# Performance work log

Measured on AMD Instinct MI355X. Metric: run time of the kernel, lower is better.

The kernel has to match this reference:

```python
import jax, jax.numpy as jnp
import numpy as np


def _round_ste(v):
    # straight-through rounding (typical LinearQuantize autograd STE)
    return v + jax.lax.stop_gradient(jnp.round(v) - v)


def setup_inputs() -> dict:
    key = jax.random.key(0)
    k1, k2, k3 = jax.random.split(key, 3)
    tokens, d_in, d_out = 8192, 2048, 2048
    x = jax.random.uniform(k1, (tokens, d_in), dtype=jnp.float32)  # non-negative acts
    weight = jax.random.normal(k2, (d_out, d_in), dtype=jnp.float32) * 0.02
    bias = jax.random.normal(k3, (d_out,), dtype=jnp.float32) * 0.02
    return {"x": x, "weight": weight, "bias": bias, "weight_bit": 8}


def reference(x, weight, bias, weight_bit):
    n = 2 ** weight_bit
    # stats computed on detached data (x.data/w.data in torch)
    wd = jax.lax.stop_gradient(weight)
    w_min = wd.min(axis=1)                      # [out]
    w_max = wd.max(axis=1)                      # [out]
    x_max = jax.lax.stop_gradient(x).max()
    scale_x = (n - 1) / jnp.clip(x_max, 1e-8)
    # activation quantization: round(scale_x * x - 0)
    q_x = _round_ste(scale_x * x)               # [T, in]
    # per-channel asymmetric weight quant (quantize_int)
    scale_w = (n - 1) / jnp.clip(w_max - w_min, 1e-8)   # [out]
    zp_w = scale_w * w_min                      # [out]
    q_w = _round_ste(scale_w[:, None] * weight - zp_w[:, None])  # [out, in]
    # bias quantized with combined scale, then clamped
    q_b = jnp.clip(_round_ste(bias * scale_w * scale_x), -n - 1, n)  # [out]
    # fake-int GEMM + zero-point correction + rescale
    mult = jnp.einsum('ti,oi->to', q_x, q_w) + q_b      # [T, out]
    res = mult + zp_w * q_x.sum(-1, keepdims=True)
    return res / scale_x / scale_w
```

## Files before the change

### kernel.cpp

```cpp
#include <hip/hip_runtime.h>
#include <stdint.h>

typedef __attribute__((ext_vector_type(4))) int i32x4;

__device__ inline float wave_max(float v){ for(int o=32;o;o>>=1) v=fmaxf(v,__shfl_xor(v,o)); return v; }
__device__ inline float wave_min(float v){ for(int o=32;o;o>>=1) v=fminf(v,__shfl_xor(v,o)); return v; }
__device__ inline int   wave_sum(int v){ for(int o=32;o;o>>=1) v+=__shfl_xor(v,o); return v; }

__device__ inline void gload16(const void* g, void* l){
  __builtin_amdgcn_global_load_lds((const __attribute__((address_space(1))) char*)g,
                                   (__attribute__((address_space(3))) char*)l, 16, 0, 0);
}

__global__ void k_xmax_partial(const float* __restrict__ x, long long n4,
                               float* __restrict__ partials){
  long long i = (long long)blockIdx.x*blockDim.x + threadIdx.x;
  long long stride = (long long)gridDim.x*blockDim.x;
  const float4* x4 = (const float4*)x;
  float m = 0.f;
  for(; i < n4; i += stride){
    float4 v = x4[i];
    m = fmaxf(m, fmaxf(fmaxf(v.x,v.y),fmaxf(v.z,v.w)));
  }
  m = wave_max(m);
  __shared__ float sm[4];
  int lane = threadIdx.x & 63, wid = threadIdx.x >> 6;
  if(lane==0) sm[wid] = m;
  __syncthreads();
  if(threadIdx.x==0)
    partials[blockIdx.x] = fmaxf(fmaxf(sm[0],sm[1]),fmaxf(sm[2],sm[3]));
}

__global__ void k_xmax_final(const float* __restrict__ partials, int nPart,
                             uint32_t* __restrict__ xmax_bits){
  float m = 0.f;
  for(int i = threadIdx.x; i < nPart; i += 256) m = fmaxf(m, partials[i]);
  m = wave_max(m);
  __shared__ float sm[4];
  int lane = threadIdx.x & 63, wid = threadIdx.x >> 6;
  if(lane==0) sm[wid] = m;
  __syncthreads();
  if(threadIdx.x==0)
    *xmax_bits = __float_as_uint(fmaxf(fmaxf(sm[0],sm[1]),fmaxf(sm[2],sm[3])));
}

__global__ void k_wstat(const float* __restrict__ w, const float* __restrict__ bias,
                        const int* __restrict__ wbit, const uint32_t* __restrict__ xmax_bits,
                        float* __restrict__ scale_w, float* __restrict__ zp_w,
                        float* __restrict__ winv,
                        int* __restrict__ cint, char* __restrict__ qw, int din){
  int row = blockIdx.x, tid = threadIdx.x;
  int lane = tid & 63, wid = tid >> 6;
  const float4* wr4 = (const float4*)(w + (long long)row*din);
  float4 a = wr4[tid*2], b = wr4[tid*2+1];
  float v[8] = {a.x,a.y,a.z,a.w,b.x,b.y,b.z,b.w};
  float mn = v[0], mx = v[0];
  for(int j=1;j<8;j++){ mn=fminf(mn,v[j]); mx=fmaxf(mx,v[j]); }
  float wmn = wave_min(mn), wmx = wave_max(mx);
  __shared__ float smn[4], smx[4];
  __shared__ float s_sw, s_zp; __shared__ int s_qb;
  if(lane==0){ smn[wid]=wmn; smx[wid]=wmx; }
  __syncthreads();
  if(tid==0){
    float fmn = fminf(fminf(smn[0],smn[1]),fminf(smn[2],smn[3]));
    float fmx = fmaxf(fmaxf(smx[0],smx[1]),fmaxf(smx[2],smx[3]));
    int n = 1 << *wbit;
    float nm1 = (float)(n-1);
    float xmax = __uint_as_float(*xmax_bits);
    float sx = __fdiv_rn(nm1, fmaxf(xmax, 1e-8f));
    float rng = __fsub_rn(fmx, fmn);
    float rngc = fmaxf(rng, 1e-8f);
    float sw = __fdiv_rn(nm1, rngc);
    float zp = __fmul_rn(sw, fmn);
    float qbf = rintf(__fmul_rn(__fmul_rn(bias[row], sw), sx));
    qbf = fminf(fmaxf(qbf, -(float)(n+1)), (float)n);
    s_sw = sw; s_zp = zp; s_qb = (int)qbf;
    scale_w[row] = sw; zp_w[row] = zp;
    winv[row] = __fdiv_rn(rngc, nm1);
  }
  __syncthreads();
  float sw = s_sw, zp = s_zp;
  int qsum = 0; uint32_t lo = 0, hi = 0;
  for(int j=0;j<8;j++){
    int q = (int)rintf(__fsub_rn(__fmul_rn(sw, v[j]), zp));
    qsum += q;
    uint32_t u = (uint32_t)((q - 128) & 0xff);
    if(j<4) lo |= u << (8*j); else hi |= u << (8*(j-4));
  }
  uint32_t* qrow = (uint32_t*)(qw + (long long)row*din);
  qrow[tid*2] = lo; qrow[tid*2+1] = hi;
  int wsum = wave_sum(qsum);
  __shared__ int ssum[4];
  if(lane==0) ssum[wid] = wsum;
  __syncthreads();
  if(tid==0){
    int Sb = ssum[0]+ssum[1]+ssum[2]+ssum[3];
    cint[row] = 128*Sb - 128*128*din + s_qb;
  }
}

__global__ void k_xquant(const float* __restrict__ x, const int* __restrict__ wbit,
                         const uint32_t* __restrict__ xmax_bits,
                         char* __restrict__ qx, int* __restrict__ Sa, int din){
  int row = blockIdx.x, tid = threadIdx.x;
  int lane = tid & 63, wid = tid >> 6;
  int n = 1 << *wbit;
  float nm1 = (float)(n-1);
  float sx = __fdiv_rn(nm1, fmaxf(__uint_as_float(*xmax_bits), 1e-8f));
  const float4* xr4 = (const float4*)(x + (long long)row*din);
  float4 a = xr4[tid*2], b = xr4[tid*2+1];
  float v[8] = {a.x,a.y,a.z,a.w,b.x,b.y,b.z,b.w};
  int qsum = 0; uint32_t lo = 0, hi = 0;
  for(int j=0;j<8;j++){
    int q = (int)rintf(__fmul_rn(sx, v[j]));
    qsum += q;
    uint32_t u = (uint32_t)((q - 128) & 0xff);
    if(j<4) lo |= u << (8*j); else hi |= u << (8*(j-4));
  }
  uint32_t* qrow = (uint32_t*)(qx + (long long)row*din);
  qrow[tid*2] = lo; qrow[tid*2+1] = hi;
  int wsum = wave_sum(qsum);
  __shared__ int ssum[4];
  if(lane==0) ssum[wid] = wsum;
  __syncthreads();
  if(tid==0) Sa[row] = ssum[0]+ssum[1]+ssum[2]+ssum[3];
}

#define TILE_BYTES 16384

__global__ __launch_bounds__(512, 2) void k_gemm(
    const char* __restrict__ qx, const char* __restrict__ qw,
    const int* __restrict__ Sa, const int* __restrict__ cint,
    const float* __restrict__ winv, const float* __restrict__ zp_w,
    const int* __restrict__ wbit, const uint32_t* __restrict__ xmax_bits,
    float* __restrict__ out, int T, int dout, int din){
  extern __shared__ char lds[];
  const int tid = threadIdx.x, lane = tid & 63, wid = tid >> 6;
  const int wr = wid >> 2, wc = wid & 3;
  const int tileN = blockIdx.x, tileM = blockIdx.y;

  const int r0 = tid >> 2,        c2s = tid & 3;
  const int r1 = (tid + 512) >> 2;
  const int sc0 = c2s ^ ((r0 >> 1) & 3);
  const int sc1 = c2s ^ ((r1 >> 1) & 3);
  const char* aG0 = qx + ((long long)tileM*256 + r0)*din + sc0*16;
  const char* aG1 = qx + ((long long)tileM*256 + r1)*din + sc1*16;
  const char* bG0 = qw + ((long long)tileN*256 + r0)*din + sc0*16;
  const char* bG1 = qw + ((long long)tileN*256 + r1)*din + sc1*16;
  const int ld0 = tid*16, ld1 = (tid+512)*16;

  const int physo = (((lane >> 4) ^ ((lane >> 1) & 3)) * 16);
  const int arowL = wr*128 + (lane & 15);
  const int browL = wc*64  + (lane & 15);

  i32x4 acc[8][4] = {};
  const int nk = din / 64;

  {
    char* A0 = lds;               char* B0 = lds + 3*TILE_BYTES;
    char* A1 = lds + TILE_BYTES;  char* B1 = lds + 4*TILE_BYTES;
    gload16(aG0, A0 + ld0); gload16(aG1, A0 + ld1);
    gload16(bG0, B0 + ld0); gload16(bG1, B0 + ld1);
    gload16(aG0 + 64, A1 + ld0); gload16(aG1 + 64, A1 + ld1);
    gload16(bG0 + 64, B1 + ld0); gload16(bG1 + 64, B1 + ld1);
  }
  asm volatile("s_waitcnt vmcnt(4)" ::: "memory");
  __builtin_amdgcn_s_barrier();

  for(int kt = 0; kt < nk; ++kt){
    const int slot  = kt % 3;
    char* As = lds + slot*TILE_BYTES;
    char* Bs = lds + (3 + slot)*TILE_BYTES;
    const bool pref = (kt + 2 < nk);
    const int nslot = (kt + 2) % 3;
    const long long ko = (long long)(kt + 2) * 64;

    i32x4 a[4], b[4];
    #pragma unroll
    for(int ni=0; ni<4; ++ni) b[ni] = *(const i32x4*)(Bs + (browL + ni*16)*64 + physo);
    #pragma unroll
    for(int mi=0; mi<4; ++mi) a[mi] = *(const i32x4*)(As + (arowL + mi*16)*64 + physo);
    if(pref){
      char* An = lds + nslot*TILE_BYTES;
      gload16(aG0 + ko, An + ld0); gload16(aG1 + ko, An + ld1);
    }
    __builtin_amdgcn_s_barrier();
    __builtin_amdgcn_s_setprio(1);
    #pragma unroll
    for(int mi=0; mi<4; ++mi)
      #pragma unroll
      for(int ni=0; ni<4; ++ni)
        acc[mi][ni] = __builtin_amdgcn_mfma_i32_16x16x64_i8(a[mi], b[ni], acc[mi][ni], 0, 0, 0);
    __builtin_amdgcn_s_setprio(0);
    __builtin_amdgcn_s_barrier();

    #pragma unroll
    for(int mi=0; mi<4; ++mi) a[mi] = *(const i32x4*)(As + (arowL + 64 + mi*16)*64 + physo);
    if(pref){
      char* Bn = lds + (3 + nslot)*TILE_BYTES;
      gload16(bG0 + ko, Bn + ld0); gload16(bG1 + ko, Bn + ld1);
    }
    __builtin_amdgcn_s_barrier();
    __builtin_amdgcn_s_setprio(1);
    #pragma unroll
    for(int mi=0; mi<4; ++mi)
      #pragma unroll
      for(int ni=0; ni<4; ++ni)
        acc[4+mi][ni] = __builtin_amdgcn_mfma_i32_16x16x64_i8(a[mi], b[ni], acc[4+mi][ni], 0, 0, 0);
    __builtin_amdgcn_s_setprio(0);
    if(kt < nk - 2) asm volatile("s_waitcnt vmcnt(4)" ::: "memory");
    else            asm volatile("s_waitcnt vmcnt(0)" ::: "memory");
    __builtin_amdgcn_s_barrier();
  }

  const float nm1 = (float)((1 << *wbit) - 1);
  const float xmaxc = fmaxf(__uint_as_float(*xmax_bits), 1e-8f);
  const float inv_sx = __fdiv_rn(xmaxc, nm1);
  const int colL = tileN*256 + wc*64 + (lane & 15);
  const int rowL = tileM*256 + wr*128 + ((lane >> 4) * 4);
  float invc[4], zp4[4]; int ci4[4];
  #pragma unroll
  for(int ni=0; ni<4; ++ni){
    int o = colL + ni*16;
    invc[ni] = __fmul_rn(winv[o], inv_sx);
    zp4[ni]  = zp_w[o];
    ci4[ni]  = cint[o];
  }
  #pragma unroll
  for(int mi=0; mi<8; ++mi){
    int rb = rowL + mi*16;
    int sav[4];
    #pragma unroll
    for(int r=0; r<4; ++r) sav[r] = Sa[rb + r];
    #pragma unroll
    for(int ni=0; ni<4; ++ni){
      #pragma unroll
      for(int r=0; r<4; ++r){
        int iv = acc[mi][ni][r] + 128*sav[r] + ci4[ni];
        float f = (float)iv + zp4[ni]*(float)sav[r];
        out[(long long)(rb + r)*dout + colL + ni*16] = __fmul_rn(f, invc[ni]);
      }
    }
  }
}

extern "C" void kernel_launch(void* const* d_in, const int* in_sizes, int n_in,
                              void* d_out, int out_size, void* d_ws, size_t ws_size,
                              hipStream_t stream){
  const float* x    = (const float*)d_in[0];
  const float* w    = (const float*)d_in[1];
  const float* bias = (const float*)d_in[2];
  const int*   wbit = (const int*)d_in[3];
  int dout = in_sizes[2];
  int din  = in_sizes[1] / dout;
  int T    = in_sizes[0] / din;

  const int NPART = 2048;
  char* ws = (char*)d_ws;
  uint32_t* xmax_bits = (uint32_t*)ws;
  size_t off = 256;
  float* partials = (float*)(ws + off); off += 4*(size_t)NPART;
  float* scale_w = (float*)(ws + off); off += 4*(size_t)dout;
  float* zp_w    = (float*)(ws + off); off += 4*(size_t)dout;
  float* winv    = (float*)(ws + off); off += 4*(size_t)dout;
  int*   cint    = (int*)(ws + off);   off += 4*(size_t)dout;
  int*   Sa      = (int*)(ws + off);   off += 4*(size_t)T;
  off = (off + 255) & ~(size_t)255;
  char*  qw      = ws + off;           off += (size_t)dout*din;
  char*  qx      = ws + off;           off += (size_t)T*din;

  long long n4 = (long long)T*din/4;
  k_xmax_partial<<<NPART, 256, 0, stream>>>(x, n4, partials);
  k_xmax_final<<<1, 256, 0, stream>>>(partials, NPART, xmax_bits);
  k_wstat<<<dout, 256, 0, stream>>>(w, bias, wbit, xmax_bits, scale_w, zp_w, winv, cint, qw, din);
  k_xquant<<<T, 256, 0, stream>>>(x, wbit, xmax_bits, qx, Sa, din);
  dim3 grid(dout/256, T/256);
  k_gemm<<<grid, 512, 6*TILE_BYTES, stream>>>(qx, qw, Sa, cint, winv, zp_w, wbit, xmax_bits,
                                              (float*)d_out, T, dout, din);
}
```

Before: 81.01 us.

## Shrink GEMM block tile to 256x128 with 4 waves and one barrier per k-step

Changes the int8 GEMM block from 256x256 with 8 waves to 256x128 with 4 waves, doubling the grid. Each k-step now issues all prefetch loads up front, then does a single LDS fragment load and 32 MFMAs per wave, behind one barrier instead of the previous split half-steps with four barriers. This cuts synchronisation overhead and gives more blocks for occupancy and load balance across CUs. In exchange, each A tile is loaded twice as many times overall, so global and LDS traffic per output rises, and each wave now holds eight A fragments in registers at once.

```diff
diff --git a/kernel.cpp b/kernel.cpp
--- a/kernel.cpp
+++ b/kernel.cpp
@@ -126,9 +126,11 @@
   if(tid==0) Sa[row] = ssum[0]+ssum[1]+ssum[2]+ssum[3];
 }
 
-#define TILE_BYTES 16384
-
-__global__ __launch_bounds__(512, 2) void k_gemm(
+#define ASLOT 16384
+#define BSLOT 8192
+#define SLOT  (ASLOT + BSLOT)
+
+__global__ __launch_bounds__(256, 2) void k_gemm(
     const char* __restrict__ qx, const char* __restrict__ qw,
     const int* __restrict__ Sa, const int* __restrict__ cint,
     const float* __restrict__ winv, const float* __restrict__ zp_w,
@@ -136,79 +138,75 @@
     float* __restrict__ out, int T, int dout, int din){
   extern __shared__ char lds[];
   const int tid = threadIdx.x, lane = tid & 63, wid = tid >> 6;
-  const int wr = wid >> 2, wc = wid & 3;
+  const int wr = (wid >> 1) * 128, wc = (wid & 1) * 64;
   const int tileN = blockIdx.x, tileM = blockIdx.y;
 
-  const int r0 = tid >> 2,        c2s = tid & 3;
-  const int r1 = (tid + 512) >> 2;
-  const int sc0 = c2s ^ ((r0 >> 1) & 3);
-  const int sc1 = c2s ^ ((r1 >> 1) & 3);
-  const char* aG0 = qx + ((long long)tileM*256 + r0)*din + sc0*16;
-  const char* aG1 = qx + ((long long)tileM*256 + r1)*din + sc1*16;
-  const char* bG0 = qw + ((long long)tileN*256 + r0)*din + sc0*16;
-  const char* bG1 = qw + ((long long)tileN*256 + r1)*din + sc1*16;
-  const int ld0 = tid*16, ld1 = (tid+512)*16;
+  const int rbase = tid >> 2, c2 = tid & 3;
+  const char* aG[4]; const char* bG[2]; int ldA[4], ldB[2];
+  #pragma unroll
+  for(int j=0;j<4;j++){
+    int row = j*64 + rbase;
+    int sc = c2 ^ ((row >> 1) & 3);
+    aG[j] = qx + ((long long)tileM*256 + row)*din + sc*16;
+    ldA[j] = (j*256 + tid)*16;
+  }
+  #pragma unroll
+  for(int j=0;j<2;j++){
+    int row = j*64 + rbase;
+    int sc = c2 ^ ((row >> 1) & 3);
+    bG[j] = qw + ((long long)tileN*128 + row)*din + sc*16;
+    ldB[j] = ASLOT + (j*256 + tid)*16;
+  }
 
   const int physo = (((lane >> 4) ^ ((lane >> 1) & 3)) * 16);
-  const int arowL = wr*128 + (lane & 15);
-  const int browL = wc*64  + (lane & 15);
+  const int arowL = wr + (lane & 15);
+  const int browL = wc + (lane & 15);
 
   i32x4 acc[8][4] = {};
   const int nk = din / 64;
 
   {
-    char* A0 = lds;               char* B0 = lds + 3*TILE_BYTES;
-    char* A1 = lds + TILE_BYTES;  char* B1 = lds + 4*TILE_BYTES;
-    gload16(aG0, A0 + ld0); gload16(aG1, A0 + ld1);
-    gload16(bG0, B0 + ld0); gload16(bG1, B0 + ld1);
-    gload16(aG0 + 64, A1 + ld0); gload16(aG1 + 64, A1 + ld1);
-    gload16(bG0 + 64, B1 + ld0); gload16(bG1 + 64, B1 + ld1);
-  }
-  asm volatile("s_waitcnt vmcnt(4)" ::: "memory");
+    char* s0 = lds; char* s1 = lds + SLOT;
+    #pragma unroll
+    for(int j=0;j<4;j++) gload16(aG[j], s0 + ldA[j]);
+    #pragma unroll
+    for(int j=0;j<2;j++) gload16(bG[j], s0 + ldB[j]);
+    #pragma unroll
+    for(int j=0;j<4;j++) gload16(aG[j] + 64, s1 + ldA[j]);
+    #pragma unroll
+    for(int j=0;j<2;j++) gload16(bG[j] + 64, s1 + ldB[j]);
+  }
+  asm volatile("s_waitcnt vmcnt(6)" ::: "memory");
   __builtin_amdgcn_s_barrier();
 
   for(int kt = 0; kt < nk; ++kt){
-    const int slot  = kt % 3;
-    char* As = lds + slot*TILE_BYTES;
-    char* Bs = lds + (3 + slot)*TILE_BYTES;
-    const bool pref = (kt + 2 < nk);
-    const int nslot = (kt + 2) % 3;
-    const long long ko = (long long)(kt + 2) * 64;
-
-    i32x4 a[4], b[4];
-    #pragma unroll
-    for(int ni=0; ni<4; ++ni) b[ni] = *(const i32x4*)(Bs + (browL + ni*16)*64 + physo);
-    #pragma unroll
-    for(int mi=0; mi<4; ++mi) a[mi] = *(const i32x4*)(As + (arowL + mi*16)*64 + physo);
-    if(pref){
-      char* An = lds + nslot*TILE_BYTES;
-      gload16(aG0 + ko, An + ld0); gload16(aG1 + ko, An + ld1);
+    char* As = lds + (kt % 3)*SLOT;
+    char* Bs = As + ASLOT;
+
+    if(kt + 2 < nk){
+      char* Sn = lds + ((kt + 2) % 3)*SLOT;
+      const long long ko = (long long)(kt + 2) * 64;
+      #pragma unroll
+      for(int j=0;j<4;j++) gload16(aG[j] + ko, Sn + ldA[j]);
+      #pragma unroll
+      for(int j=0;j<2;j++) gload16(bG[j] + ko, Sn + ldB[j]);
     }
-    __builtin_amdgcn_s_barrier();
+
+    i32x4 bf[4], af[8];
+    #pragma unroll
+    for(int ni=0; ni<4; ++ni) bf[ni] = *(const i32x4*)(Bs + (browL + ni*16)*64 + physo);
+    #pragma unroll
+    for(int mi=0; mi<8; ++mi) af[mi] = *(const i32x4*)(As + (arowL + mi*16)*64 + physo);
+
     __builtin_amdgcn_s_setprio(1);
     #pragma unroll
-    for(int mi=0; mi<4; ++mi)
+    for(int mi=0; mi<8; ++mi)
       #pragma unroll
       for(int ni=0; ni<4; ++ni)
-        acc[mi][ni] = __builtin_amdgcn_mfma_i32_16x16x64_i8(a[mi], b[ni], acc[mi][ni], 0, 0, 0);
+        acc[mi][ni] = __builtin_amdgcn_mfma_i32_16x16x64_i8(af[mi], bf[ni], acc[mi][ni], 0, 0, 0);
     __builtin_amdgcn_s_setprio(0);
-    __builtin_amdgcn_s_barrier();
-
-    #pragma unroll
-    for(int mi=0; mi<4; ++mi) a[mi] = *(const i32x4*)(As + (arowL + 64 + mi*16)*64 + physo);
-    if(pref){
-      char* Bn = lds + (3 + nslot)*TILE_BYTES;
-      gload16(bG0 + ko, Bn + ld0); gload16(bG1 + ko, Bn + ld1);
-    }
-    __builtin_amdgcn_s_barrier();
-    __builtin_amdgcn_s_setprio(1);
-    #pragma unroll
-    for(int mi=0; mi<4; ++mi)
-      #pragma unroll
-      for(int ni=0; ni<4; ++ni)
-        acc[4+mi][ni] = __builtin_amdgcn_mfma_i32_16x16x64_i8(a[mi], b[ni], acc[4+mi][ni], 0, 0, 0);
-    __builtin_amdgcn_s_setprio(0);
-    if(kt < nk - 2) asm volatile("s_waitcnt vmcnt(4)" ::: "memory");
+
+    if(kt < nk - 2) asm volatile("s_waitcnt vmcnt(6)" ::: "memory");
     else            asm volatile("s_waitcnt vmcnt(0)" ::: "memory");
     __builtin_amdgcn_s_barrier();
   }
@@ -216,8 +214,8 @@
   const float nm1 = (float)((1 << *wbit) - 1);
   const float xmaxc = fmaxf(__uint_as_float(*xmax_bits), 1e-8f);
   const float inv_sx = __fdiv_rn(xmaxc, nm1);
-  const int colL = tileN*256 + wc*64 + (lane & 15);
-  const int rowL = tileM*256 + wr*128 + ((lane >> 4) * 4);
+  const int colL = tileN*128 + wc + (lane & 15);
+  const int rowL = tileM*256 + wr + ((lane >> 4) * 4);
   float invc[4], zp4[4]; int ci4[4];
   #pragma unroll
   for(int ni=0; ni<4; ++ni){
@@ -274,7 +272,7 @@
   k_xmax_final<<<1, 256, 0, stream>>>(partials, NPART, xmax_bits);
   k_wstat<<<dout, 256, 0, stream>>>(w, bias, wbit, xmax_bits, scale_w, zp_w, winv, cint, qw, din);
   k_xquant<<<T, 256, 0, stream>>>(x, wbit, xmax_bits, qx, Sa, din);
-  dim3 grid(dout/256, T/256);
-  k_gemm<<<grid, 512, 6*TILE_BYTES, stream>>>(qx, qw, Sa, cint, winv, zp_w, wbit, xmax_bits,
-                                              (float*)d_out, T, dout, din);
-}
+  dim3 grid(dout/128, T/256);
+  k_gemm<<<grid, 256, 3*SLOT, stream>>>(qx, qw, Sa, cint, winv, zp_w, wbit, xmax_bits,
+                                        (float*)d_out, T, dout, din);
+}
```

Result: no change. 82.03 us (+1.3%).

## Restructure int8 GEMM to double-buffered 128-wide K tiles and fuse bias quant

Applied to the files above, without the earlier changes.

The GEMM main loop moves from a triple-buffered 64-byte K pipeline to a double-buffered 128-byte K pipeline using 128 KB of LDS. Each tile is consumed in four phases, and the prefetch of the next tile is interleaved across them. Bias quantization is moved out of the weight-stats kernel into the GEMM epilogue, so the weight-stats kernel no longer depends on the activation max. The restructure aims to cut loop overhead and improve load/compute overlap, at the cost of a larger LDS footprint and more barriers per K step.

```diff
diff --git a/kernel.cpp b/kernel.cpp
--- a/kernel.cpp
+++ b/kernel.cpp
@@ -44,8 +44,8 @@
     *xmax_bits = __float_as_uint(fmaxf(fmaxf(sm[0],sm[1]),fmaxf(sm[2],sm[3])));
 }
 
-__global__ void k_wstat(const float* __restrict__ w, const float* __restrict__ bias,
-                        const int* __restrict__ wbit, const uint32_t* __restrict__ xmax_bits,
+__global__ void k_wstat(const float* __restrict__ w,
+                        const int* __restrict__ wbit,
                         float* __restrict__ scale_w, float* __restrict__ zp_w,
                         float* __restrict__ winv,
                         int* __restrict__ cint, char* __restrict__ qw, int din){
@@ -58,7 +58,7 @@
   for(int j=1;j<8;j++){ mn=fminf(mn,v[j]); mx=fmaxf(mx,v[j]); }
   float wmn = wave_min(mn), wmx = wave_max(mx);
   __shared__ float smn[4], smx[4];
-  __shared__ float s_sw, s_zp; __shared__ int s_qb;
+  __shared__ float s_sw, s_zp;
   if(lane==0){ smn[wid]=wmn; smx[wid]=wmx; }
   __syncthreads();
   if(tid==0){
@@ -66,15 +66,10 @@
     float fmx = fmaxf(fmaxf(smx[0],smx[1]),fmaxf(smx[2],smx[3]));
     int n = 1 << *wbit;
     float nm1 = (float)(n-1);
-    float xmax = __uint_as_float(*xmax_bits);
-    float sx = __fdiv_rn(nm1, fmaxf(xmax, 1e-8f));
-    float rng = __fsub_rn(fmx, fmn);
-    float rngc = fmaxf(rng, 1e-8f);
+    float rngc = fmaxf(__fsub_rn(fmx, fmn), 1e-8f);
     float sw = __fdiv_rn(nm1, rngc);
     float zp = __fmul_rn(sw, fmn);
-    float qbf = rintf(__fmul_rn(__fmul_rn(bias[row], sw), sx));
-    qbf = fminf(fmaxf(qbf, -(float)(n+1)), (float)n);
-    s_sw = sw; s_zp = zp; s_qb = (int)qbf;
+    s_sw = sw; s_zp = zp;
     scale_w[row] = sw; zp_w[row] = zp;
     winv[row] = __fdiv_rn(rngc, nm1);
   }
@@ -95,7 +90,7 @@
   __syncthreads();
   if(tid==0){
     int Sb = ssum[0]+ssum[1]+ssum[2]+ssum[3];
-    cint[row] = 128*Sb - 128*128*din + s_qb;
+    cint[row] = 128*Sb - 128*128*din;
   }
 }
 
@@ -126,95 +121,85 @@
   if(tid==0) Sa[row] = ssum[0]+ssum[1]+ssum[2]+ssum[3];
 }
 
-#define TILE_BYTES 16384
-
 __global__ __launch_bounds__(512, 2) void k_gemm(
     const char* __restrict__ qx, const char* __restrict__ qw,
     const int* __restrict__ Sa, const int* __restrict__ cint,
-    const float* __restrict__ winv, const float* __restrict__ zp_w,
+    const float* __restrict__ scale_w, const float* __restrict__ winv,
+    const float* __restrict__ zp_w, const float* __restrict__ bias,
     const int* __restrict__ wbit, const uint32_t* __restrict__ xmax_bits,
     float* __restrict__ out, int T, int dout, int din){
   extern __shared__ char lds[];
   const int tid = threadIdx.x, lane = tid & 63, wid = tid >> 6;
   const int wr = wid >> 2, wc = wid & 3;
   const int tileN = blockIdx.x, tileM = blockIdx.y;
-
-  const int r0 = tid >> 2,        c2s = tid & 3;
-  const int r1 = (tid + 512) >> 2;
-  const int sc0 = c2s ^ ((r0 >> 1) & 3);
-  const int sc1 = c2s ^ ((r1 >> 1) & 3);
-  const char* aG0 = qx + ((long long)tileM*256 + r0)*din + sc0*16;
-  const char* aG1 = qx + ((long long)tileM*256 + r1)*din + sc1*16;
-  const char* bG0 = qw + ((long long)tileN*256 + r0)*din + sc0*16;
-  const char* bG1 = qw + ((long long)tileN*256 + r1)*din + sc1*16;
-  const int ld0 = tid*16, ld1 = (tid+512)*16;
+  const int nt = din / 128;
+
+  const int i0 = tid, i1 = tid + 512;
+  const int r0 = i0 >> 2, r1 = i1 >> 2;
+  const int sc0 = ((i0 & 3) ^ ((r0 >> 1) & 3)) * 16;
+  const int sc1 = ((i1 & 3) ^ ((r1 >> 1) & 3)) * 16;
+  const char* aS0 = qx + ((long long)tileM*256 + r0)*din + sc0;
+  const char* aS1 = qx + ((long long)tileM*256 + r1)*din + sc1;
+  const char* bS0 = qw + ((long long)tileN*256 + r0)*din + sc0;
+  const char* bS1 = qw + ((long long)tileN*256 + r1)*din + sc1;
+  const int d0 = i0*16, d1 = i1*16;
 
   const int physo = (((lane >> 4) ^ ((lane >> 1) & 3)) * 16);
   const int arowL = wr*128 + (lane & 15);
   const int browL = wc*64  + (lane & 15);
 
   i32x4 acc[8][4] = {};
-  const int nk = din / 64;
-
-  {
-    char* A0 = lds;               char* B0 = lds + 3*TILE_BYTES;
-    char* A1 = lds + TILE_BYTES;  char* B1 = lds + 4*TILE_BYTES;
-    gload16(aG0, A0 + ld0); gload16(aG1, A0 + ld1);
-    gload16(bG0, B0 + ld0); gload16(bG1, B0 + ld1);
-    gload16(aG0 + 64, A1 + ld0); gload16(aG1 + 64, A1 + ld1);
-    gload16(bG0 + 64, B1 + ld0); gload16(bG1 + 64, B1 + ld1);
-  }
+  i32x4 af[4], bf[4];
+
+#define STAGE_A(KS, KOFF, NB) do{ \
+    gload16(aS0 + (KOFF) + (KS)*64, (NB) + (KS)*16384 + d0); \
+    gload16(aS1 + (KOFF) + (KS)*64, (NB) + (KS)*16384 + d1); }while(0)
+#define STAGE_B(KS, KOFF, NB) do{ \
+    gload16(bS0 + (KOFF) + (KS)*64, (NB) + 32768 + (KS)*16384 + d0); \
+    gload16(bS1 + (KOFF) + (KS)*64, (NB) + 32768 + (KS)*16384 + d1); }while(0)
+
+  STAGE_A(0, 0, lds); STAGE_B(0, 0, lds);
+  STAGE_A(1, 0, lds); STAGE_B(1, 0, lds);
   asm volatile("s_waitcnt vmcnt(4)" ::: "memory");
   __builtin_amdgcn_s_barrier();
 
-  for(int kt = 0; kt < nk; ++kt){
-    const int slot  = kt % 3;
-    char* As = lds + slot*TILE_BYTES;
-    char* Bs = lds + (3 + slot)*TILE_BYTES;
-    const bool pref = (kt + 2 < nk);
-    const int nslot = (kt + 2) % 3;
-    const long long ko = (long long)(kt + 2) * 64;
-
-    i32x4 a[4], b[4];
-    #pragma unroll
-    for(int ni=0; ni<4; ++ni) b[ni] = *(const i32x4*)(Bs + (browL + ni*16)*64 + physo);
-    #pragma unroll
-    for(int mi=0; mi<4; ++mi) a[mi] = *(const i32x4*)(As + (arowL + mi*16)*64 + physo);
-    if(pref){
-      char* An = lds + nslot*TILE_BYTES;
-      gload16(aG0 + ko, An + ld0); gload16(aG1 + ko, An + ld1);
-    }
-    __builtin_amdgcn_s_barrier();
-    __builtin_amdgcn_s_setprio(1);
-    #pragma unroll
-    for(int mi=0; mi<4; ++mi)
-      #pragma unroll
-      for(int ni=0; ni<4; ++ni)
-        acc[mi][ni] = __builtin_amdgcn_mfma_i32_16x16x64_i8(a[mi], b[ni], acc[mi][ni], 0, 0, 0);
-    __builtin_amdgcn_s_setprio(0);
-    __builtin_amdgcn_s_barrier();
-
-    #pragma unroll
-    for(int mi=0; mi<4; ++mi) a[mi] = *(const i32x4*)(As + (arowL + 64 + mi*16)*64 + physo);
-    if(pref){
-      char* Bn = lds + (3 + nslot)*TILE_BYTES;
-      gload16(bG0 + ko, Bn + ld0); gload16(bG1 + ko, Bn + ld1);
-    }
-    __builtin_amdgcn_s_barrier();
-    __builtin_amdgcn_s_setprio(1);
-    #pragma unroll
-    for(int mi=0; mi<4; ++mi)
-      #pragma unroll
-      for(int ni=0; ni<4; ++ni)
-        acc[4+mi][ni] = __builtin_amdgcn_mfma_i32_16x16x64_i8(a[mi], b[ni], acc[4+mi][ni], 0, 0, 0);
-    __builtin_amdgcn_s_setprio(0);
-    if(kt < nk - 2) asm volatile("s_waitcnt vmcnt(4)" ::: "memory");
-    else            asm volatile("s_waitcnt vmcnt(0)" ::: "memory");
-    __builtin_amdgcn_s_barrier();
-  }
-
-  const float nm1 = (float)((1 << *wbit) - 1);
+  for(int t = 0; t < nt; ++t){
+    char* Ab = lds + (t & 1)*65536;
+    char* Bb = Ab + 32768;
+    char* NB = lds + ((t & 1)^1)*65536;
+    const bool ld = (t + 1 < nt);
+    const int koff = (t + 1)*128;
+
+#define PH(MH, KS, DO_B, STAGE_STMT, VM_STMT) do{ \
+    if(DO_B){ _Pragma("unroll") \
+      for(int ni=0;ni<4;++ni) bf[ni] = *(const i32x4*)(Bb + (KS)*16384 + (browL + ni*16)*64 + physo); } \
+    _Pragma("unroll") \
+    for(int mi=0;mi<4;++mi) af[mi] = *(const i32x4*)(Ab + (KS)*16384 + (arowL + (MH)*64 + mi*16)*64 + physo); \
+    STAGE_STMT; \
+    __builtin_amdgcn_s_barrier(); \
+    __builtin_amdgcn_s_setprio(1); \
+    _Pragma("unroll") \
+    for(int mi=0;mi<4;++mi){ _Pragma("unroll") \
+      for(int ni=0;ni<4;++ni) \
+        acc[(MH)*4+mi][ni] = __builtin_amdgcn_mfma_i32_16x16x64_i8(af[mi], bf[ni], acc[(MH)*4+mi][ni], 0,0,0); } \
+    __builtin_amdgcn_s_setprio(0); \
+    VM_STMT; \
+    __builtin_amdgcn_s_barrier(); }while(0)
+
+    PH(0, 0, true,  if(ld) STAGE_A(0, koff, NB), );
+    PH(1, 0, false, if(ld) STAGE_B(0, koff, NB),
+       if(ld){ asm volatile("s_waitcnt vmcnt(4)" ::: "memory"); }
+       else  { asm volatile("s_waitcnt vmcnt(0)" ::: "memory"); });
+    PH(0, 1, true,  if(ld) STAGE_A(1, koff, NB), );
+    PH(1, 1, false, if(ld) STAGE_B(1, koff, NB),
+       if(ld){ asm volatile("s_waitcnt vmcnt(4)" ::: "memory"); });
+#undef PH
+  }
+
+  const int n = 1 << *wbit;
+  const float nm1 = (float)(n-1);
   const float xmaxc = fmaxf(__uint_as_float(*xmax_bits), 1e-8f);
+  const float sx = __fdiv_rn(nm1, xmaxc);
   const float inv_sx = __fdiv_rn(xmaxc, nm1);
   const int colL = tileN*256 + wc*64 + (lane & 15);
   const int rowL = tileM*256 + wr*128 + ((lane >> 4) * 4);
@@ -222,9 +207,12 @@
   #pragma unroll
   for(int ni=0; ni<4; ++ni){
     int o = colL + ni*16;
+    float sw = scale_w[o];
+    float qbf = rintf(__fmul_rn(__fmul_rn(bias[o], sw), sx));
+    qbf = fminf(fmaxf(qbf, -(float)(n+1)), (float)n);
+    ci4[ni] = cint[o] + (int)qbf;
     invc[ni] = __fmul_rn(winv[o], inv_sx);
     zp4[ni]  = zp_w[o];
-    ci4[ni]  = cint[o];
   }
   #pragma unroll
   for(int mi=0; mi<8; ++mi){
@@ -272,9 +260,9 @@
   long long n4 = (long long)T*din/4;
   k_xmax_partial<<<NPART, 256, 0, stream>>>(x, n4, partials);
   k_xmax_final<<<1, 256, 0, stream>>>(partials, NPART, xmax_bits);
-  k_wstat<<<dout, 256, 0, stream>>>(w, bias, wbit, xmax_bits, scale_w, zp_w, winv, cint, qw, din);
+  k_wstat<<<dout, 256, 0, stream>>>(w, wbit, scale_w, zp_w, winv, cint, qw, din);
   k_xquant<<<T, 256, 0, stream>>>(x, wbit, xmax_bits, qx, Sa, din);
   dim3 grid(dout/256, T/256);
-  k_gemm<<<grid, 512, 6*TILE_BYTES, stream>>>(qx, qw, Sa, cint, winv, zp_w, wbit, xmax_bits,
-                                              (float*)d_out, T, dout, din);
-}
+  k_gemm<<<grid, 512, 131072, stream>>>(qx, qw, Sa, cint, scale_w, winv, zp_w, bias,
+                                        wbit, xmax_bits, (float*)d_out, T, dout, din);
+}
```

Result: no change. 80.34 us (-0.8%).
